# Performance work log

Measured on AMD Instinct MI355X. Metric: run time of the kernel, lower is better.

## Reference

```python
import jax, jax.numpy as jnp
import numpy as np

EPS = 1e-5
NUM_HEADS = 8

def _inorm(x):
    # InstanceNorm1d (affine=False): normalize over last (length) axis per (B, C)
    m = x.mean(axis=-1, keepdims=True)
    v = x.var(axis=-1, keepdims=True)  # biased variance, as torch instance norm
    return (x - m) * jax.lax.rsqrt(v + EPS)

def setup_inputs() -> dict:
    key = jax.random.key(0)
    ks = jax.random.split(key, 12)
    B, Nl, HW = 4, 1024, 4096
    Cl, Cv, Ck, Cval, Cout = 512, 512, 256, 256, 256
    w = lambda k, shape: (jax.random.normal(k, shape, jnp.float32) * 0.02)
    return {
        "l": jax.random.normal(ks[0], (B, Nl, Cl), jnp.float32),
        "x": jax.random.normal(ks[1], (B, HW, Cv), jnp.float32),
        "Wq": w(ks[2], (Ck, Cl)),   "bq": w(ks[3], (Ck,)),
        "Wk": w(ks[4], (Ck, Cv)),   "bk": w(ks[5], (Ck,)),
        "Wv": w(ks[6], (Cval, Cv)), "bv": w(ks[7], (Cval,)),
        "Ww": w(ks[8], (Cout, Cval)), "bw": w(ks[9], (Cout,)),
    }

def reference(l, x, Wq, bq, Wk, bk, Wv, bv, Ww, bw):
    H = NUM_HEADS
    Ck = Wq.shape[0]
    Cv = Wv.shape[0]
    dk, dv = Ck // H, Cv // H
    B, Nl, _ = l.shape
    HW = x.shape[1]

    # 1x1 Conv1d == per-position linear
    q = jnp.einsum('blc,kc->blk', l, Wq) + bq                     # [B, Nl, Ck]
    k = jnp.einsum('bnc,kc->bkn', x, Wk) + bk[None, :, None]      # [B, Ck, HW]
    k = _inorm(k)                                                  # InstanceNorm over HW
    v = jnp.einsum('bnc,kc->bkn', x, Wv) + bv[None, :, None]      # [B, Cv, HW]

    q = q.reshape(B, Nl, H, dk).transpose(0, 2, 1, 3)             # [B, H, Nl, dk]
    k = k.reshape(B, H, dk, HW)                                   # [B, H, dk, HW]
    v = v.reshape(B, H, dv, HW)                                   # [B, H, dv, HW]

    sim = jnp.einsum('bhld,bhdn->bhln', q, k) * (Ck ** -0.5)      # [B, H, Nl, HW]
    att = jax.nn.softmax(sim, axis=-1)
    out = jnp.einsum('bhln,bhdn->bhld', att, v)                   # [B, H, Nl, dv]

    out = out.transpose(0, 2, 1, 3).reshape(B, Nl, Cv)            # [B, Nl, Cv]
    out = jnp.einsum('blc,oc->bol', out, Ww) + bw[None, :, None]  # [B, Cout, Nl]
    out = _inorm(out)                                              # InstanceNorm over Nl
    return out.transpose(0, 2, 1)                                  # [B, Nl, Cout]
```

## Files before the change

kernel.cpp:

```cpp
#include <hip/hip_runtime.h>

constexpr int Bn = 4, NL = 1024, HWn = 4096, NH = 8;

typedef __attribute__((ext_vector_type(8))) short bf16x8;
typedef __attribute__((ext_vector_type(4))) float f32x4;
#define MFMA16 __builtin_amdgcn_mfma_f32_16x16x32_bf16

extern "C" __device__ float __ocml_native_exp2_f32(float);

__device__ __forceinline__ float b2f(unsigned short u) {
  union { unsigned int i; float f; } x; x.i = ((unsigned int)u) << 16; return x.f;
}
__device__ __forceinline__ unsigned short f2b(float f) {
  union { float f; unsigned int i; } x; x.f = f;
  unsigned int r = x.i + 0x7fffu + ((x.i >> 16) & 1u);
  return (unsigned short)(r >> 16);
}

__device__ __forceinline__ void async_load16(const unsigned short* g, unsigned short* l) {
  __builtin_amdgcn_global_load_lds(
      (const __attribute__((address_space(1))) unsigned int*)g,
      (__attribute__((address_space(3))) unsigned int*)l, 16, 0, 0);
}

__global__ __launch_bounds__(256) void convall(const float* __restrict__ x,
    const float* __restrict__ l,
    const float* __restrict__ Wk, const float* __restrict__ Wv,
    const float* __restrict__ Wq, const float* __restrict__ Ww,
    unsigned short* __restrict__ xbf, unsigned short* __restrict__ lbf,
    unsigned short* __restrict__ wkb, unsigned short* __restrict__ wvb,
    unsigned short* __restrict__ wqb,
    unsigned short* __restrict__ wwh, unsigned short* __restrict__ wwl,
    float* __restrict__ Fz)
{
  const int id = blockIdx.x, tid = threadIdx.x;
  if (id < 8192) {
    int i = (id * 256 + tid) * 4;
    float4 v = *(const float4*)(x + i);
    ushort4 o; o.x = f2b(v.x); o.y = f2b(v.y); o.z = f2b(v.z); o.w = f2b(v.w);
    *(ushort4*)(xbf + i) = o;
  } else if (id < 10240) {
    int i = ((id - 8192) * 256 + tid) * 4;
    float4 v = *(const float4*)(l + i);
    ushort4 o; o.x = f2b(v.x); o.y = f2b(v.y); o.z = f2b(v.z); o.w = f2b(v.w);
    *(ushort4*)(lbf + i) = o;
  } else if (id < 10752) {
    int sub = id - 10240;
    int y = sub >> 7, bx = sub & 127;
    int i = (bx * 256 + tid) * 4;
    if (y == 3) {
      if (i >= 65536) return;
      float4 v = *(const float4*)(Ww + i);
      ushort4 hi, lo;
      hi.x = f2b(v.x); lo.x = f2b(v.x - b2f(hi.x));
      hi.y = f2b(v.y); lo.y = f2b(v.y - b2f(hi.y));
      hi.z = f2b(v.z); lo.z = f2b(v.z - b2f(hi.z));
      hi.w = f2b(v.w); lo.w = f2b(v.w - b2f(hi.w));
      *(ushort4*)(wwh + i) = hi;
      *(ushort4*)(wwl + i) = lo;
      return;
    }
    const float* src = y == 0 ? Wk : (y == 1 ? Wv : Wq);
    unsigned short* dst = y == 0 ? wkb : (y == 1 ? wvb : wqb);
    float4 v = *(const float4*)(src + i);
    ushort4 o; o.x = f2b(v.x); o.y = f2b(v.y); o.z = f2b(v.z); o.w = f2b(v.w);
    *(ushort4*)(dst + i) = o;
  } else {
    int i = (id - 10752) * 1024 + tid * 4;
    *(float4*)(Fz + i) = (float4){0.f, 0.f, 0.f, 0.f};
  }
}

__global__ __launch_bounds__(256, 3) void gemm128(
    const unsigned short* __restrict__ xbf, const unsigned short* __restrict__ lbf,
    const unsigned short* __restrict__ wkb, const unsigned short* __restrict__ wvb,
    const unsigned short* __restrict__ wqb,
    const float* __restrict__ bk, const float* __restrict__ bv, const float* __restrict__ bq,
    unsigned short* __restrict__ khb, unsigned short* __restrict__ vhb,
    unsigned short* __restrict__ qbuf,
    float* __restrict__ ksum, float* __restrict__ kss, float* __restrict__ vcs)
{
  __shared__ unsigned short As[2][4096];
  __shared__ unsigned short Bs[2][4096];
  const int id = blockIdx.x;
  const int mode = id < 256 ? 0 : (id < 512 ? 1 : 2);
  const int local = id - (mode == 0 ? 0 : (mode == 1 ? 256 : 512));
  const int rb = local >> 1, cb = local & 1;
  const int m0 = rb * 128, n0 = cb * 128;
  const unsigned short* A = (mode == 2) ? lbf : xbf;
  const unsigned short* W = (mode == 0) ? wkb : (mode == 1 ? wvb : wqb);
  const float* bias = (mode == 0) ? bk : (mode == 1 ? bv : bq);

  const int tid = threadIdx.x, w = tid >> 6, lane = tid & 63;
  const int quad = lane >> 4, l15 = lane & 15;
  const int wr = w >> 1, wc = w & 1;

  const int p0 = tid, p1 = tid + 256;
  const int am0 = p0 >> 2, ak0 = (p0 & 3) * 8;
  const int am1 = p1 >> 2, ak1 = (p1 & 3) * 8;

  f32x4 acc[4][4];
#pragma unroll
  for (int i = 0; i < 4; ++i)
#pragma unroll
    for (int j = 0; j < 4; ++j) acc[i][j] = (f32x4){0.f, 0.f, 0.f, 0.f};

  async_load16(A + (size_t)(m0 + am0) * 512 + ak0, &As[0][p0 * 8]);
  async_load16(A + (size_t)(m0 + am1) * 512 + ak1, &As[0][p1 * 8]);
  async_load16(W + (size_t)(n0 + am0) * 512 + ak0, &Bs[0][p0 * 8]);
  async_load16(W + (size_t)(n0 + am1) * 512 + ak1, &Bs[0][p1 * 8]);

  for (int kt = 0; kt < 16; ++kt) {
    const int cur = kt & 1;
    __syncthreads();
    if (kt < 15) {
      int k0 = (kt + 1) * 32;
      async_load16(A + (size_t)(m0 + am0) * 512 + k0 + ak0, &As[cur ^ 1][p0 * 8]);
      async_load16(A + (size_t)(m0 + am1) * 512 + k0 + ak1, &As[cur ^ 1][p1 * 8]);
      async_load16(W + (size_t)(n0 + am0) * 512 + k0 + ak0, &Bs[cur ^ 1][p0 * 8]);
      async_load16(W + (size_t)(n0 + am1) * 512 + k0 + ak1, &Bs[cur ^ 1][p1 * 8]);
    }
    bf16x8 af[4], bf[4];
#pragma unroll
    for (int fr = 0; fr < 4; ++fr)
      af[fr] = *(const bf16x8*)&As[cur][(wr * 64 + fr * 16 + l15) * 32 + quad * 8];
#pragma unroll
    for (int fc = 0; fc < 4; ++fc)
      bf[fc] = *(const bf16x8*)&Bs[cur][(wc * 64 + fc * 16 + l15) * 32 + quad * 8];
#pragma unroll
    for (int fr = 0; fr < 4; ++fr)
#pragma unroll
      for (int fc = 0; fc < 4; ++fc)
        acc[fr][fc] = MFMA16(af[fr], bf[fc], acc[fr][fc], 0, 0, 0);
  }

  float bb[4];
#pragma unroll
  for (int fc = 0; fc < 4; ++fc) bb[fc] = bias[n0 + wc * 64 + fc * 16 + l15];

  if (mode != 2) {
    const int b = m0 >> 12;
    const int seg = (m0 & 4095) >> 9;
#pragma unroll
    for (int fc = 0; fc < 4; ++fc) {
      float s = 0.f, ssq = 0.f;
#pragma unroll
      for (int fr = 0; fr < 4; ++fr)
#pragma unroll
        for (int r = 0; r < 4; ++r) {
          float v = acc[fr][fc][r] + bb[fc];
          s += v; ssq += v * v;
        }
      s += __shfl_xor(s, 16); s += __shfl_xor(s, 32);
      if (mode == 0) {
        ssq += __shfl_xor(ssq, 16); ssq += __shfl_xor(ssq, 32);
        if (quad == 0) {
          int col = n0 + wc * 64 + fc * 16 + l15;
          atomicAdd(&ksum[b * 256 + col], s);
          atomicAdd(&kss[b * 256 + col], ssq);
        }
      } else if (quad == 0) {
        int col = n0 + wc * 64 + fc * 16 + l15;
        atomicAdd(&vcs[seg * 1024 + b * 256 + col], s);
      }
    }
  }

  unsigned short* dst = (mode == 0) ? khb : (mode == 1 ? vhb : qbuf);
#pragma unroll
  for (int fr = 0; fr < 4; ++fr) {
#pragma unroll
    for (int fc = 0; fc < 4; ++fc) {
      int col = n0 + wc * 64 + fc * 16 + l15;
#pragma unroll
      for (int r = 0; r < 4; ++r) {
        int row = m0 + wr * 64 + fr * 16 + quad * 4 + r;
        unsigned short val = f2b(acc[fr][fc][r] + bb[fc]);
        if (mode == 2) {
          dst[(size_t)row * 256 + col] = val;
        } else {
          int b = row >> 12, n = row & 4095, h = col >> 5, d = col & 31;
          dst[((size_t)(b * 8 + h) * 4096 + n) * 32 + d] = val;
        }
      }
    }
  }
}

__global__ __launch_bounds__(256) void vpack(const unsigned short* __restrict__ vh,
    unsigned short* __restrict__ vfrag)
{
  __shared__ unsigned short vt[256][42];
  const int bh = blockIdx.x >> 4, slab = blockIdx.x & 15;
  const unsigned short* src = vh + ((size_t)bh * 4096 + slab * 256) * 32;
  const int t = threadIdx.x;
#pragma unroll
  for (int i = 0; i < 4; ++i) {
    int p = i * 256 + t;
    int n = p >> 2, piece = p & 3;
    uint4 v = *(const uint4*)(src + (size_t)n * 32 + piece * 8);
    unsigned int* lrow = (unsigned int*)&vt[n][piece * 8];
    lrow[0] = v.x; lrow[1] = v.y; lrow[2] = v.z; lrow[3] = v.w;
  }
  __syncthreads();
#pragma unroll
  for (int i = 0; i < 4; ++i) {
    int op = i * 256 + t;
    int lanep = op & 63, rest = op >> 6;
    int dvt = rest & 1, kh2 = (rest >> 1) & 1, chunkl = rest >> 2;
    int lq = lanep >> 4, ll = lanep & 15;
    unsigned short o[8];
#pragma unroll
    for (int j = 0; j < 8; ++j) {
      int kappa = kh2 * 32 + lq * 8 + j;
      int nloc = (kappa >> 2) + 16 * (kappa & 3);
      o[j] = vt[chunkl * 64 + nloc][dvt * 16 + ll];
    }
    size_t dst = ((((size_t)bh * 64 + slab * 4 + chunkl) * 2 + kh2) * 2 + dvt) * 512 + lanep * 8;
    *(bf16x8*)(vfrag + dst) = *(const bf16x8*)o;
  }
}

__global__ __launch_bounds__(256, 4) void attn8(const unsigned short* __restrict__ qbuf,
    const unsigned short* __restrict__ khb, const unsigned short* __restrict__ vfrag,
    const float* __restrict__ ksum, const float* __restrict__ kss,
    const float* __restrict__ vcs,
    float* __restrict__ po, float* __restrict__ pd)
{
  const int bh = blockIdx.x, b = bh >> 3, h = bh & 7;
  const int lsuper = blockIdx.y, quarter = blockIdx.z;
  const int tid = threadIdx.x, w = tid >> 6, lane = tid & 63;
  const int quad = lane >> 4, l15 = lane & 15;

  __shared__ unsigned short kb_s[2][2048];
  __shared__ unsigned short vb_s[2][2048];
  __shared__ unsigned short ps[4][2][16][64];

  bf16x8 qa[2];
  {
    float fold[8];
    const int ch = bh * 32 + quad * 8;
#pragma unroll
    for (int j = 0; j < 8; ++j) {
      float m = ksum[ch + j] * (1.f / 4096.f);
      float var = kss[ch + j] * (1.f / 4096.f) - m * m;
      fold[j] = rsqrtf(var + 1e-5f) * (0.0625f * 1.44269504f);
    }
#pragma unroll
    for (int lf = 0; lf < 2; ++lf) {
      int l = lsuper * 128 + w * 32 + lf * 16 + l15;
      bf16x8 qr = *(const bf16x8*)(qbuf + ((size_t)(b * NL + l)) * 256 + h * 32 + quad * 8);
      const unsigned short* qq = (const unsigned short*)&qr;
      unsigned short tmp[8];
#pragma unroll
      for (int j = 0; j < 8; ++j) tmp[j] = f2b(b2f(qq[j]) * fold[j]);
      qa[lf] = *(const bf16x8*)tmp;
    }
  }

  float drow[2][4];
  f32x4 acc[2][2];
#pragma unroll
  for (int lf = 0; lf < 2; ++lf) {
#pragma unroll
    for (int r = 0; r < 4; ++r) drow[lf][r] = 0.f;
    acc[lf][0] = (f32x4){0.f,0.f,0.f,0.f};
    acc[lf][1] = (f32x4){0.f,0.f,0.f,0.f};
  }

  const unsigned short* kcbase = khb + (size_t)bh * 131072 + (size_t)quarter * 1024 * 32;
  const unsigned short* vcbase = vfrag + (size_t)bh * 131072 + (size_t)quarter * 16 * 2048;

  async_load16(kcbase + tid * 8, &kb_s[0][tid * 8]);
  async_load16(vcbase + tid * 8, &vb_s[0][tid * 8]);

  unsigned short* psw = &ps[w][0][0][0];
  const unsigned rdswz = (unsigned)((l15 & 7) << 4);

  for (int c = 0; c < 16; ++c) {
    const int cur = c & 1;
    __syncthreads();
    if (c < 15) {
      async_load16(kcbase + (c + 1) * 2048 + tid * 8, &kb_s[cur ^ 1][tid * 8]);
      async_load16(vcbase + (c + 1) * 2048 + tid * 8, &vb_s[cur ^ 1][tid * 8]);
    }

    bf16x8 kb[4];
#pragma unroll
    for (int t = 0; t < 4; ++t)
      kb[t] = *(const bf16x8*)&kb_s[cur][(t * 16 + l15) * 32 + quad * 8];
    bf16x8 vb[4];
#pragma unroll
    for (int i = 0; i < 4; ++i)
      vb[i] = *(const bf16x8*)&vb_s[cur][i * 512 + lane * 8];

    const f32x4 z = (f32x4){0.f,0.f,0.f,0.f};
#pragma unroll
    for (int lf = 0; lf < 2; ++lf) {
      f32x4 sv[4];
#pragma unroll
      for (int t = 0; t < 4; ++t) sv[t] = MFMA16(qa[lf], kb[t], z, 0, 0, 0);
#pragma unroll
      for (int r = 0; r < 4; ++r) {
        float x0 = __ocml_native_exp2_f32(sv[0][r]);
        float x1 = __ocml_native_exp2_f32(sv[1][r]);
        float x2 = __ocml_native_exp2_f32(sv[2][r]);
        float x3 = __ocml_native_exp2_f32(sv[3][r]);
        drow[lf][r] += (x0 + x1) + (x2 + x3);
        unsigned pk0, pk1;
        asm("v_cvt_pk_bf16_f32 %0, %1, %2" : "=v"(pk0) : "v"(x0 - 1.0f), "v"(x1 - 1.0f));
        asm("v_cvt_pk_bf16_f32 %0, %1, %2" : "=v"(pk1) : "v"(x2 - 1.0f), "v"(x3 - 1.0f));
        const int row = quad * 4 + r;
        unsigned off = (unsigned)((l15 * 8) ^ ((row & 7) << 4));
        uint2 pk; pk.x = pk0; pk.y = pk1;
        *(uint2*)((char*)(psw + lf * 1024 + row * 64) + off) = pk;
      }
      asm volatile("s_waitcnt lgkmcnt(0)" ::: "memory");
#pragma unroll
      for (int kh2 = 0; kh2 < 2; ++kh2) {
        unsigned off = (unsigned)((kh2 * 64 + quad * 16) ^ rdswz);
        bf16x8 pa = *(const bf16x8*)((const char*)(psw + lf * 1024 + l15 * 64) + off);
        acc[lf][0] = MFMA16(pa, vb[kh2 * 2 + 0], acc[lf][0], 0, 0, 0);
        acc[lf][1] = MFMA16(pa, vb[kh2 * 2 + 1], acc[lf][1], 0, 0, 0);
      }
    }
  }

  const float* vc0 = vcs + (quarter * 2) * 1024 + bh * 32;
  const float* vc1 = vc0 + 1024;
  float cs0 = vc0[l15] + vc1[l15];
  float cs1 = vc0[16 + l15] + vc1[16 + l15];
#pragma unroll
  for (int lf = 0; lf < 2; ++lf)
#pragma unroll
    for (int r = 0; r < 4; ++r) {
      acc[lf][0][r] += cs0;
      acc[lf][1][r] += cs1;
    }

  const size_t PDo = (size_t)quarter * 32768 + (size_t)bh * 1024;
#pragma unroll
  for (int lf = 0; lf < 2; ++lf) {
#pragma unroll
    for (int r = 0; r < 4; ++r) {
      float sv = drow[lf][r];
      sv += __shfl_xor(sv, 1, 16);
      sv += __shfl_xor(sv, 2, 16);
      sv += __shfl_xor(sv, 4, 16);
      sv += __shfl_xor(sv, 8, 16);
      int l = lsuper * 128 + w * 32 + lf * 16 + quad * 4 + r;
      float2 val; val.x = acc[lf][0][r]; val.y = acc[lf][1][r];
      *(float2*)(po + (PDo + l) * 32 + l15 * 2) = val;
      if (l15 == 0) pd[PDo + l] = sv;
    }
  }
}

__global__ __launch_bounds__(256) void combine4(const float* __restrict__ po,
    const float* __restrict__ pd, unsigned short* __restrict__ aoh,
    unsigned short* __restrict__ aol)
{
  int gid = blockIdx.x * 256 + threadIdx.x;
  int dv = gid & 31, l = (gid >> 5) & (NL - 1), h = (gid >> 15) & 7, b = gid >> 18;
  int c = ((dv & 15) << 1) | (dv >> 4);
  size_t r = ((size_t)(b * 8 + h)) * 1024 + l;
  float d = 0.f, o = 0.f;
#pragma unroll
  for (int q = 0; q < 4; ++q) {
    size_t rr = (size_t)q * 32768 + r;
    d += pd[rr];
    o += po[rr * 32 + c];
  }
  o = o / d;
  unsigned short hi = f2b(o);
  size_t idx = ((size_t)(b * NL) + l) * 256 + h * 32 + dv;
  aoh[idx] = hi;
  aol[idx] = f2b(o - b2f(hi));
}

__global__ __launch_bounds__(256) void gemm_proj(
    const unsigned short* __restrict__ aoh, const unsigned short* __restrict__ aol,
    const unsigned short* __restrict__ wwh, const unsigned short* __restrict__ wwl,
    const float* __restrict__ bw, float* __restrict__ pj,
    float* __restrict__ psum, float* __restrict__ psq)
{
  __shared__ unsigned short As[64 * 32];
  __shared__ unsigned short Bs[64 * 32];
  const int bm = blockIdx.x * 64, bn = blockIdx.y * 64;
  const int tid = threadIdx.x, w = tid >> 6, lane = tid & 63;
  const int quad = lane >> 4, l15 = lane & 15;
  const int wr = w >> 1, wc = w & 1;
  const int arow = tid >> 2, apiece = (tid & 3) * 8;

  f32x4 acc[2][2];
#pragma unroll
  for (int i = 0; i < 2; ++i)
#pragma unroll
    for (int j = 0; j < 2; ++j) acc[i][j] = (f32x4){0.f, 0.f, 0.f, 0.f};

  for (int pair = 0; pair < 3; ++pair) {
    const unsigned short* A = (pair == 1) ? aol : aoh;
    const unsigned short* Bm = (pair == 2) ? wwl : wwh;
    for (int kt = 0; kt < 8; ++kt) {
      int k0 = kt * 32;
      __syncthreads();
      *(bf16x8*)&As[tid * 8] = *(const bf16x8*)(A + (size_t)(bm + arow) * 256 + k0 + apiece);
      *(bf16x8*)&Bs[tid * 8] = *(const bf16x8*)(Bm + (size_t)(bn + arow) * 256 + k0 + apiece);
      __syncthreads();
      bf16x8 af[2], bf[2];
#pragma unroll
      for (int fr = 0; fr < 2; ++fr)
        af[fr] = *(const bf16x8*)&As[(wr * 32 + fr * 16 + l15) * 32 + quad * 8];
#pragma unroll
      for (int fc = 0; fc < 2; ++fc)
        bf[fc] = *(const bf16x8*)&Bs[(wc * 32 + fc * 16 + l15) * 32 + quad * 8];
#pragma unroll
      for (int fr = 0; fr < 2; ++fr)
#pragma unroll
        for (int fc = 0; fc < 2; ++fc)
          acc[fr][fc] = MFMA16(af[fr], bf[fc], acc[fr][fc], 0, 0, 0);
    }
  }

  const int b = bm >> 10;
#pragma unroll
  for (int fr = 0; fr < 2; ++fr)
#pragma unroll
    for (int fc = 0; fc < 2; ++fc) {
      int col = bn + wc * 32 + fc * 16 + l15;
      float bb = bw[col];
      float s = 0.f, ssq = 0.f;
#pragma unroll
      for (int r = 0; r < 4; ++r) {
        int row = bm + wr * 32 + fr * 16 + quad * 4 + r;
        float v = acc[fr][fc][r] + bb;
        pj[(size_t)row * 256 + col] = v;
        s += v; ssq += v * v;
      }
      s += __shfl_xor(s, 16); s += __shfl_xor(s, 32);
      ssq += __shfl_xor(ssq, 16); ssq += __shfl_xor(ssq, 32);
      if (quad == 0) {
        atomicAdd(&psum[b * 256 + col], s);
        atomicAdd(&psq[b * 256 + col], ssq);
      }
    }
}

__global__ __launch_bounds__(256) void final_out(const float* __restrict__ proj,
    const float* __restrict__ psum, const float* __restrict__ psq,
    float* __restrict__ out)
{
  const int b = blockIdx.x, o = threadIdx.x;
  const int l1 = blockIdx.y * 16;
  const float m = psum[b * 256 + o] * (1.f / 1024.f);
  const float r = rsqrtf(psq[b * 256 + o] * (1.f / 1024.f) - m * m + 1e-5f);
  for (int i = 0; i < 16; ++i) {
    size_t idx = ((size_t)(b * NL + l1 + i)) * 256 + o;
    out[idx] = (proj[idx] - m) * r;
  }
}

extern "C" void kernel_launch(void* const* d_in, const int* in_sizes, int n_in,
                              void* d_out, int out_size, void* d_ws, size_t ws_size,
                              hipStream_t stream)
{
  const float* l  = (const float*)d_in[0];
  const float* x  = (const float*)d_in[1];
  const float* Wq = (const float*)d_in[2];
  const float* bq = (const float*)d_in[3];
  const float* Wk = (const float*)d_in[4];
  const float* bk = (const float*)d_in[5];
  const float* Wv = (const float*)d_in[6];
  const float* bv = (const float*)d_in[7];
  const float* Ww = (const float*)d_in[8];
  const float* bw = (const float*)d_in[9];
  float* out = (float*)d_out;

  unsigned short* up = (unsigned short*)d_ws;
  unsigned short* xbf   = up;
  unsigned short* lbf   = xbf   + 8388608;
  unsigned short* wkb   = lbf   + 2097152;
  unsigned short* wvb   = wkb   + 131072;
  unsigned short* wqb   = wvb   + 131072;
  unsigned short* qbuf  = wqb   + 131072;
  unsigned short* khb   = qbuf  + 1048576;
  unsigned short* vhb   = khb   + 4194304;
  unsigned short* vfrag = vhb   + 4194304;
  unsigned short* aoh   = vfrag + 4194304;
  unsigned short* aol   = aoh   + 1048576;
  unsigned short* wwh   = aol   + 1048576;
  unsigned short* wwl   = wwh   + 65536;
  float* F     = (float*)((char*)d_ws + 53477376);
  float* ksum  = F;
  float* kss   = F + 1024;
  float* vcs   = F + 2048;
  float* psum  = F + 10240;
  float* psq   = F + 11264;
  float* po    = F + 15360;
  float* pd    = po + 4194304;
  float* pj    = po;

  dim3 blk(256);
  convall<<<10764, blk, 0, stream>>>(x, l, Wk, Wv, Wq, Ww, xbf, lbf,
                                     wkb, wvb, wqb, wwh, wwl, F);
  gemm128<<<576, blk, 0, stream>>>(xbf, lbf, wkb, wvb, wqb, bk, bv, bq,
                                   khb, vhb, qbuf, ksum, kss, vcs);
  vpack<<<512, blk, 0, stream>>>(vhb, vfrag);
  attn8<<<dim3(32, 8, 4), blk, 0, stream>>>(qbuf, khb, vfrag, ksum, kss, vcs, po, pd);
  combine4<<<4096, blk, 0, stream>>>(po, pd, aoh, aol);
  gemm_proj<<<dim3(64, 4), blk, 0, stream>>>(aoh, aol, wwh, wwl, bw, pj, psum, psq);
  final_out<<<dim3(4, 64), blk, 0, stream>>>(pj, psum, psq, out);
}
```

Measured before the change: 179.7 us.

## Triple-buffer async LDS loads in GEMM and attention with explicit vmcnt waits

```diff
diff --git a/kernel.cpp b/kernel.cpp
--- a/kernel.cpp
+++ b/kernel.cpp
@@ -80,8 +80,8 @@
     unsigned short* __restrict__ qbuf,
     float* __restrict__ ksum, float* __restrict__ kss, float* __restrict__ vcs)
 {
-  __shared__ unsigned short As[2][4096];
-  __shared__ unsigned short Bs[2][4096];
+  __shared__ unsigned short As[3][4096];
+  __shared__ unsigned short Bs[3][4096];
   const int id = blockIdx.x;
   const int mode = id < 256 ? 0 : (id < 512 ? 1 : 2);
   const int local = id - (mode == 0 ? 0 : (mode == 1 ? 256 : 512));
@@ -105,33 +105,40 @@
 #pragma unroll
     for (int j = 0; j < 4; ++j) acc[i][j] = (f32x4){0.f, 0.f, 0.f, 0.f};
 
-  async_load16(A + (size_t)(m0 + am0) * 512 + ak0, &As[0][p0 * 8]);
-  async_load16(A + (size_t)(m0 + am1) * 512 + ak1, &As[0][p1 * 8]);
-  async_load16(W + (size_t)(n0 + am0) * 512 + ak0, &Bs[0][p0 * 8]);
-  async_load16(W + (size_t)(n0 + am1) * 512 + ak1, &Bs[0][p1 * 8]);
-
+#pragma unroll
+  for (int pk = 0; pk < 2; ++pk) {
+    int k0 = pk * 32;
+    async_load16(A + (size_t)(m0 + am0) * 512 + k0 + ak0, &As[pk][p0 * 8]);
+    async_load16(A + (size_t)(m0 + am1) * 512 + k0 + ak1, &As[pk][p1 * 8]);
+    async_load16(W + (size_t)(n0 + am0) * 512 + k0 + ak0, &Bs[pk][p0 * 8]);
+    async_load16(W + (size_t)(n0 + am1) * 512 + k0 + ak1, &Bs[pk][p1 * 8]);
+  }
+
+  int b0 = 0, b1 = 1, b2 = 2;
   for (int kt = 0; kt < 16; ++kt) {
-    const int cur = kt & 1;
-    __syncthreads();
-    if (kt < 15) {
-      int k0 = (kt + 1) * 32;
-      async_load16(A + (size_t)(m0 + am0) * 512 + k0 + ak0, &As[cur ^ 1][p0 * 8]);
-      async_load16(A + (size_t)(m0 + am1) * 512 + k0 + ak1, &As[cur ^ 1][p1 * 8]);
-      async_load16(W + (size_t)(n0 + am0) * 512 + k0 + ak0, &Bs[cur ^ 1][p0 * 8]);
-      async_load16(W + (size_t)(n0 + am1) * 512 + k0 + ak1, &Bs[cur ^ 1][p1 * 8]);
+    if (kt < 15) asm volatile("s_waitcnt vmcnt(4)" ::: "memory");
+    else         asm volatile("s_waitcnt vmcnt(0)" ::: "memory");
+    __builtin_amdgcn_s_barrier();
+    if (kt < 14) {
+      int k0 = (kt + 2) * 32;
+      async_load16(A + (size_t)(m0 + am0) * 512 + k0 + ak0, &As[b2][p0 * 8]);
+      async_load16(A + (size_t)(m0 + am1) * 512 + k0 + ak1, &As[b2][p1 * 8]);
+      async_load16(W + (size_t)(n0 + am0) * 512 + k0 + ak0, &Bs[b2][p0 * 8]);
+      async_load16(W + (size_t)(n0 + am1) * 512 + k0 + ak1, &Bs[b2][p1 * 8]);
     }
     bf16x8 af[4], bf[4];
 #pragma unroll
     for (int fr = 0; fr < 4; ++fr)
-      af[fr] = *(const bf16x8*)&As[cur][(wr * 64 + fr * 16 + l15) * 32 + quad * 8];
+      af[fr] = *(const bf16x8*)&As[b0][(wr * 64 + fr * 16 + l15) * 32 + quad * 8];
 #pragma unroll
     for (int fc = 0; fc < 4; ++fc)
-      bf[fc] = *(const bf16x8*)&Bs[cur][(wc * 64 + fc * 16 + l15) * 32 + quad * 8];
+      bf[fc] = *(const bf16x8*)&Bs[b0][(wc * 64 + fc * 16 + l15) * 32 + quad * 8];
 #pragma unroll
     for (int fr = 0; fr < 4; ++fr)
 #pragma unroll
       for (int fc = 0; fc < 4; ++fc)
         acc[fr][fc] = MFMA16(af[fr], bf[fc], acc[fr][fc], 0, 0, 0);
+    int t = b0; b0 = b1; b1 = b2; b2 = t;
   }
 
   float bb[4];
@@ -221,7 +228,7 @@
   }
 }
 
-__global__ __launch_bounds__(256, 4) void attn8(const unsigned short* __restrict__ qbuf,
+__global__ __launch_bounds__(256, 4) void attn9(const unsigned short* __restrict__ qbuf,
     const unsigned short* __restrict__ khb, const unsigned short* __restrict__ vfrag,
     const float* __restrict__ ksum, const float* __restrict__ kss,
     const float* __restrict__ vcs,
@@ -232,8 +239,8 @@
   const int tid = threadIdx.x, w = tid >> 6, lane = tid & 63;
   const int quad = lane >> 4, l15 = lane & 15;
 
-  __shared__ unsigned short kb_s[2][2048];
-  __shared__ unsigned short vb_s[2][2048];
+  __shared__ unsigned short kb_s[3][2048];
+  __shared__ unsigned short vb_s[3][2048];
   __shared__ unsigned short ps[4][2][16][64];
 
   bf16x8 qa[2];
@@ -273,33 +280,39 @@
 
   async_load16(kcbase + tid * 8, &kb_s[0][tid * 8]);
   async_load16(vcbase + tid * 8, &vb_s[0][tid * 8]);
+  async_load16(kcbase + 2048 + tid * 8, &kb_s[1][tid * 8]);
+  async_load16(vcbase + 2048 + tid * 8, &vb_s[1][tid * 8]);
 
   unsigned short* psw = &ps[w][0][0][0];
   const unsigned rdswz = (unsigned)((l15 & 7) << 4);
 
+  int b0 = 0, b1 = 1, b2 = 2;
   for (int c = 0; c < 16; ++c) {
-    const int cur = c & 1;
-    __syncthreads();
-    if (c < 15) {
-      async_load16(kcbase + (c + 1) * 2048 + tid * 8, &kb_s[cur ^ 1][tid * 8]);
-      async_load16(vcbase + (c + 1) * 2048 + tid * 8, &vb_s[cur ^ 1][tid * 8]);
+    if (c < 15) asm volatile("s_waitcnt vmcnt(2)" ::: "memory");
+    else        asm volatile("s_waitcnt vmcnt(0)" ::: "memory");
+    __builtin_amdgcn_s_barrier();
+    if (c < 14) {
+      async_load16(kcbase + (c + 2) * 2048 + tid * 8, &kb_s[b2][tid * 8]);
+      async_load16(vcbase + (c + 2) * 2048 + tid * 8, &vb_s[b2][tid * 8]);
     }
 
     bf16x8 kb[4];
 #pragma unroll
     for (int t = 0; t < 4; ++t)
-      kb[t] = *(const bf16x8*)&kb_s[cur][(t * 16 + l15) * 32 + quad * 8];
+      kb[t] = *(const bf16x8*)&kb_s[b0][(t * 16 + l15) * 32 + quad * 8];
     bf16x8 vb[4];
 #pragma unroll
     for (int i = 0; i < 4; ++i)
-      vb[i] = *(const bf16x8*)&vb_s[cur][i * 512 + lane * 8];
+      vb[i] = *(const bf16x8*)&vb_s[b0][i * 512 + lane * 8];
 
     const f32x4 z = (f32x4){0.f,0.f,0.f,0.f};
 #pragma unroll
     for (int lf = 0; lf < 2; ++lf) {
       f32x4 sv[4];
+      __builtin_amdgcn_s_setprio(1);
 #pragma unroll
       for (int t = 0; t < 4; ++t) sv[t] = MFMA16(qa[lf], kb[t], z, 0, 0, 0);
+      __builtin_amdgcn_s_setprio(0);
 #pragma unroll
       for (int r = 0; r < 4; ++r) {
         float x0 = __ocml_native_exp2_f32(sv[0][r]);
@@ -316,6 +329,7 @@
         *(uint2*)((char*)(psw + lf * 1024 + row * 64) + off) = pk;
       }
       asm volatile("s_waitcnt lgkmcnt(0)" ::: "memory");
+      __builtin_amdgcn_s_setprio(1);
 #pragma unroll
       for (int kh2 = 0; kh2 < 2; ++kh2) {
         unsigned off = (unsigned)((kh2 * 64 + quad * 16) ^ rdswz);
@@ -323,7 +337,9 @@
         acc[lf][0] = MFMA16(pa, vb[kh2 * 2 + 0], acc[lf][0], 0, 0, 0);
         acc[lf][1] = MFMA16(pa, vb[kh2 * 2 + 1], acc[lf][1], 0, 0, 0);
       }
-    }
+      __builtin_amdgcn_s_setprio(0);
+    }
+    int t = b0; b0 = b1; b1 = b2; b2 = t;
   }
 
   const float* vc0 = vcs + (quarter * 2) * 1024 + bh * 32;
@@ -506,7 +522,7 @@
   gemm128<<<576, blk, 0, stream>>>(xbf, lbf, wkb, wvb, wqb, bk, bv, bq,
                                    khb, vhb, qbuf, ksum, kss, vcs);
   vpack<<<512, blk, 0, stream>>>(vhb, vfrag);
-  attn8<<<dim3(32, 8, 4), blk, 0, stream>>>(qbuf, khb, vfrag, ksum, kss, vcs, po, pd);
+  attn9<<<dim3(32, 8, 4), blk, 0, stream>>>(qbuf, khb, vfrag, ksum, kss, vcs, po, pd);
   combine4<<<4096, blk, 0, stream>>>(po, pd, aoh, aol);
   gemm_proj<<<dim3(64, 4), blk, 0, stream>>>(aoh, aol, wwh, wwl, bw, pj, psum, psq);
   final_out<<<dim3(4, 64), blk, 0, stream>>>(pj, psum, psq, out);
```

New measurement: 179.2 us. About the same (-0.3%).

## Fuse V fragment packing into GEMM epilogue; load K/V directly from global

Applied to the files above, without the earlier changes.

```diff
diff --git a/kernel.cpp b/kernel.cpp
--- a/kernel.cpp
+++ b/kernel.cpp
@@ -76,7 +76,7 @@
     const unsigned short* __restrict__ wkb, const unsigned short* __restrict__ wvb,
     const unsigned short* __restrict__ wqb,
     const float* __restrict__ bk, const float* __restrict__ bv, const float* __restrict__ bq,
-    unsigned short* __restrict__ khb, unsigned short* __restrict__ vhb,
+    unsigned short* __restrict__ khb, unsigned short* __restrict__ vfrag,
     unsigned short* __restrict__ qbuf,
     float* __restrict__ ksum, float* __restrict__ kss, float* __restrict__ vcs)
 {
@@ -166,62 +166,49 @@
     }
   }
 
-  unsigned short* dst = (mode == 0) ? khb : (mode == 1 ? vhb : qbuf);
-#pragma unroll
-  for (int fr = 0; fr < 4; ++fr) {
+  if (mode == 1) {
+    const int b = m0 >> 12;
+    const int seg64 = ((m0 & 4095) >> 6) + wr;
 #pragma unroll
     for (int fc = 0; fc < 4; ++fc) {
       int col = n0 + wc * 64 + fc * 16 + l15;
-#pragma unroll
-      for (int r = 0; r < 4; ++r) {
-        int row = m0 + wr * 64 + fr * 16 + quad * 4 + r;
-        unsigned short val = f2b(acc[fr][fc][r] + bb[fc]);
-        if (mode == 2) {
-          dst[(size_t)row * 256 + col] = val;
-        } else {
-          int b = row >> 12, n = row & 4095, h = col >> 5, d = col & 31;
-          dst[((size_t)(b * 8 + h) * 4096 + n) * 32 + d] = val;
+      int h = col >> 5, d = col & 31;
+      int dvt = d >> 4, ll = d & 15;
+      size_t base = (size_t)((b * 8 + h) * 64 + seg64) * 2048 + dvt * 512;
+#pragma unroll
+      for (int fr = 0; fr < 4; ++fr) {
+#pragma unroll
+        for (int r = 0; r < 4; ++r) {
+          int kappa = 4 * (quad * 4 + r) + fr;
+          int kh2 = kappa >> 5, lq = (kappa >> 3) & 3, j = kappa & 7;
+          vfrag[base + kh2 * 1024 + (lq * 16 + ll) * 8 + j] = f2b(acc[fr][fc][r] + bb[fc]);
         }
       }
     }
-  }
-}
-
-__global__ __launch_bounds__(256) void vpack(const unsigned short* __restrict__ vh,
-    unsigned short* __restrict__ vfrag)
-{
-  __shared__ unsigned short vt[256][42];
-  const int bh = blockIdx.x >> 4, slab = blockIdx.x & 15;
-  const unsigned short* src = vh + ((size_t)bh * 4096 + slab * 256) * 32;
-  const int t = threadIdx.x;
-#pragma unroll
-  for (int i = 0; i < 4; ++i) {
-    int p = i * 256 + t;
-    int n = p >> 2, piece = p & 3;
-    uint4 v = *(const uint4*)(src + (size_t)n * 32 + piece * 8);
-    unsigned int* lrow = (unsigned int*)&vt[n][piece * 8];
-    lrow[0] = v.x; lrow[1] = v.y; lrow[2] = v.z; lrow[3] = v.w;
-  }
-  __syncthreads();
-#pragma unroll
-  for (int i = 0; i < 4; ++i) {
-    int op = i * 256 + t;
-    int lanep = op & 63, rest = op >> 6;
-    int dvt = rest & 1, kh2 = (rest >> 1) & 1, chunkl = rest >> 2;
-    int lq = lanep >> 4, ll = lanep & 15;
-    unsigned short o[8];
-#pragma unroll
-    for (int j = 0; j < 8; ++j) {
-      int kappa = kh2 * 32 + lq * 8 + j;
-      int nloc = (kappa >> 2) + 16 * (kappa & 3);
-      o[j] = vt[chunkl * 64 + nloc][dvt * 16 + ll];
-    }
-    size_t dst = ((((size_t)bh * 64 + slab * 4 + chunkl) * 2 + kh2) * 2 + dvt) * 512 + lanep * 8;
-    *(bf16x8*)(vfrag + dst) = *(const bf16x8*)o;
-  }
-}
-
-__global__ __launch_bounds__(256, 4) void attn8(const unsigned short* __restrict__ qbuf,
+  } else {
+    unsigned short* dst = (mode == 0) ? khb : qbuf;
+#pragma unroll
+    for (int fr = 0; fr < 4; ++fr) {
+#pragma unroll
+      for (int fc = 0; fc < 4; ++fc) {
+        int col = n0 + wc * 64 + fc * 16 + l15;
+#pragma unroll
+        for (int r = 0; r < 4; ++r) {
+          int row = m0 + wr * 64 + fr * 16 + quad * 4 + r;
+          unsigned short val = f2b(acc[fr][fc][r] + bb[fc]);
+          if (mode == 2) {
+            dst[(size_t)row * 256 + col] = val;
+          } else {
+            int b = row >> 12, n = row & 4095, h = col >> 5, d = col & 31;
+            dst[((size_t)(b * 8 + h) * 4096 + n) * 32 + d] = val;
+          }
+        }
+      }
+    }
+  }
+}
+
+__global__ __launch_bounds__(256, 4) void attn10(const unsigned short* __restrict__ qbuf,
     const unsigned short* __restrict__ khb, const unsigned short* __restrict__ vfrag,
     const float* __restrict__ ksum, const float* __restrict__ kss,
     const float* __restrict__ vcs,
@@ -232,8 +219,6 @@
   const int tid = threadIdx.x, w = tid >> 6, lane = tid & 63;
   const int quad = lane >> 4, l15 = lane & 15;
 
-  __shared__ unsigned short kb_s[2][2048];
-  __shared__ unsigned short vb_s[2][2048];
   __shared__ unsigned short ps[4][2][16][64];
 
   bf16x8 qa[2];
@@ -268,38 +253,31 @@
     acc[lf][1] = (f32x4){0.f,0.f,0.f,0.f};
   }
 
-  const unsigned short* kcbase = khb + (size_t)bh * 131072 + (size_t)quarter * 1024 * 32;
-  const unsigned short* vcbase = vfrag + (size_t)bh * 131072 + (size_t)quarter * 16 * 2048;
-
-  async_load16(kcbase + tid * 8, &kb_s[0][tid * 8]);
-  async_load16(vcbase + tid * 8, &vb_s[0][tid * 8]);
+  const unsigned short* kl = khb + (size_t)bh * 131072 + (size_t)quarter * 32768
+                             + l15 * 32 + quad * 8;
+  const unsigned short* vl = vfrag + (size_t)bh * 131072 + (size_t)quarter * 32768
+                             + lane * 8;
 
   unsigned short* psw = &ps[w][0][0][0];
   const unsigned rdswz = (unsigned)((l15 & 7) << 4);
 
   for (int c = 0; c < 16; ++c) {
-    const int cur = c & 1;
-    __syncthreads();
-    if (c < 15) {
-      async_load16(kcbase + (c + 1) * 2048 + tid * 8, &kb_s[cur ^ 1][tid * 8]);
-      async_load16(vcbase + (c + 1) * 2048 + tid * 8, &vb_s[cur ^ 1][tid * 8]);
-    }
-
-    bf16x8 kb[4];
+    bf16x8 kb[4], vb[4];
 #pragma unroll
     for (int t = 0; t < 4; ++t)
-      kb[t] = *(const bf16x8*)&kb_s[cur][(t * 16 + l15) * 32 + quad * 8];
-    bf16x8 vb[4];
+      kb[t] = *(const bf16x8*)(kl + c * 2048 + t * 512);
 #pragma unroll
     for (int i = 0; i < 4; ++i)
-      vb[i] = *(const bf16x8*)&vb_s[cur][i * 512 + lane * 8];
+      vb[i] = *(const bf16x8*)(vl + c * 2048 + i * 512);
 
     const f32x4 z = (f32x4){0.f,0.f,0.f,0.f};
 #pragma unroll
     for (int lf = 0; lf < 2; ++lf) {
       f32x4 sv[4];
+      __builtin_amdgcn_s_setprio(1);
 #pragma unroll
       for (int t = 0; t < 4; ++t) sv[t] = MFMA16(qa[lf], kb[t], z, 0, 0, 0);
+      __builtin_amdgcn_s_setprio(0);
 #pragma unroll
       for (int r = 0; r < 4; ++r) {
         float x0 = __ocml_native_exp2_f32(sv[0][r]);
@@ -316,6 +294,7 @@
         *(uint2*)((char*)(psw + lf * 1024 + row * 64) + off) = pk;
       }
       asm volatile("s_waitcnt lgkmcnt(0)" ::: "memory");
+      __builtin_amdgcn_s_setprio(1);
 #pragma unroll
       for (int kh2 = 0; kh2 < 2; ++kh2) {
         unsigned off = (unsigned)((kh2 * 64 + quad * 16) ^ rdswz);
@@ -323,6 +302,7 @@
         acc[lf][0] = MFMA16(pa, vb[kh2 * 2 + 0], acc[lf][0], 0, 0, 0);
         acc[lf][1] = MFMA16(pa, vb[kh2 * 2 + 1], acc[lf][1], 0, 0, 0);
       }
+      __builtin_amdgcn_s_setprio(0);
     }
   }
 
@@ -504,9 +484,8 @@
   convall<<<10764, blk, 0, stream>>>(x, l, Wk, Wv, Wq, Ww, xbf, lbf,
                                      wkb, wvb, wqb, wwh, wwl, F);
   gemm128<<<576, blk, 0, stream>>>(xbf, lbf, wkb, wvb, wqb, bk, bv, bq,
-                                   khb, vhb, qbuf, ksum, kss, vcs);
-  vpack<<<512, blk, 0, stream>>>(vhb, vfrag);
-  attn8<<<dim3(32, 8, 4), blk, 0, stream>>>(qbuf, khb, vfrag, ksum, kss, vcs, po, pd);
+                                   khb, vfrag, qbuf, ksum, kss, vcs);
+  attn10<<<dim3(32, 8, 4), blk, 0, stream>>>(qbuf, khb, vfrag, ksum, kss, vcs, po, pd);
   combine4<<<4096, blk, 0, stream>>>(po, pd, aoh, aol);
   gemm_proj<<<dim3(64, 4), blk, 0, stream>>>(aoh, aol, wwh, wwl, bw, pj, psum, psq);
   final_out<<<dim3(4, 64), blk, 0, stream>>>(pj, psum, psq, out);
```

New measurement: 172.6 us. -3.9%, faster.
